# Performance work log

Hardware: AMD Instinct MI355X
Metric: run time of the kernel (lower is better)

## Reference

```python
import jax, jax.numpy as jnp
import numpy as np
from jax import lax

B, T, D, L = 64, 512, 1024, 32


def setup_inputs() -> dict:
    key = jax.random.key(0)
    ks = jax.random.split(key, 6)
    embeddings = jax.random.normal(ks[0], (B, T, D), dtype=jnp.float32)
    W = jax.random.normal(ks[1], (L, D), dtype=jnp.float32) * (1.0 / np.sqrt(D))
    b = jnp.zeros((L,), dtype=jnp.float32)
    start_trans = jax.random.normal(ks[2], (L,), dtype=jnp.float32) * 0.1
    end_trans = jax.random.normal(ks[3], (L,), dtype=jnp.float32) * 0.1
    trans = jax.random.normal(ks[4], (L, L), dtype=jnp.float32) * 0.1
    labels = jax.random.randint(ks[5], (B, T), 0, L, dtype=jnp.int32)
    mask = jnp.ones((B, T), dtype=bool)  # torchcrf requires mask[:, 0] == True
    return {"embeddings": embeddings, "W": W, "b": b,
            "start_trans": start_trans, "end_trans": end_trans,
            "trans": trans, "labels": labels, "mask": mask}


def _crf_nll(emissions, labels, mask, start_trans, end_trans, trans):
    # emissions: [B, T, L]; torchcrf works time-first internally.
    em = jnp.transpose(emissions, (1, 0, 2))          # [T, B, L]
    tg = labels.T                                      # [T, B]
    mk_b = mask.T                                      # [T, B] bool
    mk_f = mk_b.astype(emissions.dtype)
    bidx = jnp.arange(em.shape[1])

    # ---- numerator: score of the gold tag path ----
    score0 = start_trans[tg[0]] + em[0, bidx, tg[0]]   # [B]

    def num_step(carry, inp):
        prev_tag, score = carry
        e_t, tag_t, m_b, m_f = inp
        step = trans[prev_tag, tag_t] + e_t[bidx, tag_t]
        score = score + step * m_f
        prev_tag = jnp.where(m_b, tag_t, prev_tag)
        return (prev_tag, score), None

    (last_tag, num), _ = lax.scan(num_step, (tg[0], score0),
                                  (em[1:], tg[1:], mk_b[1:], mk_f[1:]))
    num = num + end_trans[last_tag]

    # ---- denominator: forward algorithm (log partition) ----
    alpha0 = start_trans[None, :] + em[0]              # [B, L]

    def den_step(alpha, inp):
        e_t, m_b = inp
        # alpha[b, i] + trans[i, j] + e_t[b, j] -> logsumexp over i
        nxt = jax.nn.logsumexp(alpha[:, :, None] + trans[None, :, :]
                               + e_t[:, None, :], axis=1)
        alpha = jnp.where(m_b[:, None], nxt, alpha)
        return alpha, None

    alpha, _ = lax.scan(den_step, alpha0, (em[1:], mk_b[1:]))
    den = jax.nn.logsumexp(alpha + end_trans[None, :], axis=1)  # [B]

    llh = num - den                                    # log-likelihood per seq
    return -jnp.mean(llh)                              # reduction='mean', negated


def reference(embeddings, W, b, start_trans, end_trans, trans, labels, mask):
    # dropout is identity at eval time
    emissions = jnp.einsum('btd,ld->btl', embeddings, W) + b  # [B, T, L]
    return _crf_nll(emissions, labels, mask, start_trans, end_trans, trans)
```

## Files before the change

### kernel.cpp

```cpp
#include <hip/hip_runtime.h>
#include <hip/hip_bf16.h>

#define NB 64
#define NT 512
#define ND 1024
#define NL 32
#define SEG 16
#define NSEG 32

typedef __attribute__((ext_vector_type(8)))  short bf16x8;
typedef __attribute__((ext_vector_type(4)))  float f32x4;
typedef __attribute__((ext_vector_type(16))) float f32x16;

__device__ __forceinline__ unsigned short bfh(float x) {
    __hip_bfloat16 h = __float2bfloat16(x);
    return *(unsigned short*)&h;
}
__device__ __forceinline__ float frombf(unsigned short u) {
    return __uint_as_float(((unsigned)u) << 16);
}

__global__ __launch_bounds__(256) void wb_kernel(
    const float* __restrict__ W, unsigned short* __restrict__ Wb)
{
    int i = blockIdx.x * 256 + threadIdx.x;
    float4 v = ((const float4*)W)[i];
    ushort4 o;
    o.x = bfh(v.x); o.y = bfh(v.y); o.z = bfh(v.z); o.w = bfh(v.w);
    ((ushort4*)Wb)[i] = o;
}

__global__ __launch_bounds__(256) void emis_kernel(
    const float* __restrict__ emb,
    const unsigned short* __restrict__ Wb,
    const float* __restrict__ bias,
    float* __restrict__ eme)
{
    __shared__ unsigned short As[64][80];
    const int tid  = threadIdx.x;
    const int wv   = tid >> 6;
    const int lane = tid & 63;
    const int m    = lane & 15;
    const int quad = lane >> 4;
    const int row0 = blockIdx.x * 64;

    const int srow = tid >> 4;
    const int sk4  = tid & 15;
    const float* gp = emb + (size_t)(row0 + srow) * ND + sk4 * 4;

    float4 rA[4];
#pragma unroll
    for (int q = 0; q < 4; q++) rA[q] = *(const float4*)(gp + (size_t)q * 16 * ND);

    f32x4 acc0 = {0.f, 0.f, 0.f, 0.f};
    f32x4 acc1 = {0.f, 0.f, 0.f, 0.f};

    for (int c = 0; c < 16; c++) {
        if (c) __syncthreads();
#pragma unroll
        for (int q = 0; q < 4; q++) {
            ushort4 pk;
            pk.x = bfh(rA[q].x); pk.y = bfh(rA[q].y);
            pk.z = bfh(rA[q].z); pk.w = bfh(rA[q].w);
            *(ushort4*)&As[srow + 16 * q][sk4 * 4] = pk;
        }
        __syncthreads();

        if (c < 15) {
            const float* np = gp + (c + 1) * 64;
#pragma unroll
            for (int q = 0; q < 4; q++) rA[q] = *(const float4*)(np + (size_t)q * 16 * ND);
        }

#pragma unroll
        for (int ks = 0; ks < 2; ks++) {
            int kb = c * 64 + ks * 32 + quad * 8;
            bf16x8 bf0 = *(const bf16x8*)&Wb[(size_t)m * ND + kb];
            bf16x8 bf1 = *(const bf16x8*)&Wb[(size_t)(16 + m) * ND + kb];
            bf16x8 af  = *(const bf16x8*)&As[16 * wv + m][ks * 32 + quad * 8];
            acc0 = __builtin_amdgcn_mfma_f32_16x16x32_bf16(af, bf0, acc0, 0, 0, 0);
            acc1 = __builtin_amdgcn_mfma_f32_16x16x32_bf16(af, bf1, acc1, 0, 0, 0);
        }
    }

    const int n = m;
    const float bl0 = bias[n];
    const float bl1 = bias[16 + n];
#pragma unroll
    for (int r = 0; r < 4; r++) {
        int R = row0 + 16 * wv + quad * 4 + r;
        float* op = eme + (size_t)R * NL;
        op[n]      = __expf(acc0[r] + bl0);
        op[16 + n] = __expf(acc1[r] + bl1);
    }
}

__global__ __launch_bounds__(64) void seg_kernel(
    const float* __restrict__ eme,
    const float* __restrict__ trans,
    const int*   __restrict__ labels,
    unsigned short* __restrict__ Pm,
    int*   __restrict__ exps,
    float* __restrict__ numpart)
{
    const int blk  = blockIdx.x;
    const int b    = blk >> 5;
    const int s    = blk & 31;
    const int lane = threadIdx.x;
    const int col  = lane & 31;
    const int h    = lane >> 5;
    const int t0   = s * SEG;
    const int tstart = (s == 0) ? 1 : t0;

    __shared__ __align__(16) float em_lds[SEG][NL];
    __shared__ __align__(16) unsigned short T2[2][32][40];

    {
        const float* src = eme + ((size_t)b * NT + t0) * NL;
        *(float4*)&((float*)em_lds)[lane * 8]     = *(const float4*)&src[lane * 8];
        *(float4*)&((float*)em_lds)[lane * 8 + 4] = *(const float4*)&src[lane * 8 + 4];
    }
    __syncthreads();

    {
        float npart = 0.f;
        if (lane < SEG) {
            int t = t0 + lane;
            if (t >= 1) {
                int pt = labels[b * NT + t - 1], ct = labels[b * NT + t];
                npart = trans[pt * NL + ct] + __logf(em_lds[lane][ct]);
            }
        }
#pragma unroll
        for (int mk = 32; mk >= 1; mk >>= 1) npart += __shfl_xor(npart, mk, 64);
        if (lane == 0) numpart[b * NSEG + s] = npart;
    }

    float Ecol[16];
#pragma unroll
    for (int j = 0; j < 8; j++) Ecol[j]     = __expf(trans[(8 * h + j) * NL + col]);
#pragma unroll
    for (int j = 0; j < 8; j++) Ecol[8 + j] = __expf(trans[(16 + 8 * h + j) * NL + col]);

    bf16x8 A1, A2;
    {
        const float* emt = em_lds[tstart - t0];
#pragma unroll
        for (int j = 0; j < 8; j++) {
            int k1 = 8 * h + j, k2 = 16 + 8 * h + j;
            ((unsigned short*)&A1)[j] = bfh(__expf(trans[col * NL + k1]) * emt[k1]);
            ((unsigned short*)&A2)[j] = bfh(__expf(trans[col * NL + k2]) * emt[k2]);
        }
    }

    int eseg = 0, par = 0, lastp = 0;
    for (int t = tstart + 1; t <= t0 + SEG - 1; t++) {
        float emn = em_lds[t - t0][col];
        bf16x8 B1, B2;
#pragma unroll
        for (int j = 0; j < 8; j++) {
            ((unsigned short*)&B1)[j] = bfh(Ecol[j] * emn);
            ((unsigned short*)&B2)[j] = bfh(Ecol[8 + j] * emn);
        }

        f32x16 acc;
#pragma unroll
        for (int i = 0; i < 16; i++) acc[i] = 0.f;
        acc = __builtin_amdgcn_mfma_f32_32x32x16_bf16(A1, B1, acc, 0, 0, 0);
        acc = __builtin_amdgcn_mfma_f32_32x32x16_bf16(A2, B2, acc, 0, 0, 0);

        int bits = __builtin_amdgcn_readlane(__float_as_int(acc[0]), 0);
        int e = (bits >> 23) & 255;
        eseg += e - 127;
        float scale = __uint_as_float((unsigned)(254 - e) << 23);

#pragma unroll
        for (int r = 0; r < 16; r++) {
            int row = (r & 3) + 8 * (r >> 2) + 4 * h;
            T2[par][row][col] = bfh(acc[r] * scale);
        }
        __syncthreads();
        A1 = *(const bf16x8*)&T2[par][col][8 * h];
        A2 = *(const bf16x8*)&T2[par][col][16 + 8 * h];
        lastp = par;
        par ^= 1;
    }

    if (h == 0) {
        unsigned short* dst = Pm + ((size_t)(b * NSEG + s) << 10) + col * 32;
        const uint4* srcrow = (const uint4*)&T2[lastp][col][0];
        ((uint4*)dst)[0] = srcrow[0];
        ((uint4*)dst)[1] = srcrow[1];
    }
    if (lane == 0) exps[b * NSEG + s] = eseg;
}

__global__ __launch_bounds__(64) void comb_kernel(
    const float* __restrict__ eme,
    const float* __restrict__ start_trans,
    const float* __restrict__ end_trans,
    const unsigned short* __restrict__ Pm,
    const int*   __restrict__ exps,
    const float* __restrict__ numpart,
    const int*   __restrict__ labels,
    float* __restrict__ den_out,
    float* __restrict__ num_out)
{
    const int b    = blockIdx.x;
    const int lane = threadIdx.x;
    const int col  = lane & 31;

    float a = __expf(start_trans[col]) * eme[(size_t)b * NT * NL + col];
    int sexp = 0;
    float sv[32];
#pragma unroll
    for (int i = 0; i < 32; i++)
        sv[i] = __int_as_float(__builtin_amdgcn_readlane(__float_as_int(a), i));

    const unsigned short* Pb = Pm + ((size_t)b * NSEG << 10);
    float Pc[32];
#pragma unroll
    for (int i = 0; i < 32; i++) Pc[i] = frombf(Pb[i * 32 + col]);

    for (int s = 0; s < NSEG; s++) {
        unsigned short nb[32];
        if (s + 1 < NSEG) {
            const unsigned short* q = Pb + ((s + 1) << 10);
#pragma unroll
            for (int i = 0; i < 32; i++) nb[i] = q[i * 32 + col];
        } else {
#pragma unroll
            for (int i = 0; i < 32; i++) nb[i] = 0;
        }

        float p0 = sv[0] * Pc[0], p1 = sv[1] * Pc[1];
        float p2 = sv[2] * Pc[2], p3 = sv[3] * Pc[3];
        float p4 = sv[4] * Pc[4], p5 = sv[5] * Pc[5];
        float p6 = sv[6] * Pc[6], p7 = sv[7] * Pc[7];
#pragma unroll
        for (int i = 8; i < 32; i += 8) {
            p0 = fmaf(sv[i + 0], Pc[i + 0], p0);
            p1 = fmaf(sv[i + 1], Pc[i + 1], p1);
            p2 = fmaf(sv[i + 2], Pc[i + 2], p2);
            p3 = fmaf(sv[i + 3], Pc[i + 3], p3);
            p4 = fmaf(sv[i + 4], Pc[i + 4], p4);
            p5 = fmaf(sv[i + 5], Pc[i + 5], p5);
            p6 = fmaf(sv[i + 6], Pc[i + 6], p6);
            p7 = fmaf(sv[i + 7], Pc[i + 7], p7);
        }
        a = (((p0 + p1) + (p2 + p3)) + ((p4 + p5) + (p6 + p7)));

        int bits = __builtin_amdgcn_readlane(__float_as_int(a), 0);
        int e = (bits >> 23) & 255;
        sexp += e - 127;
        a *= __uint_as_float((unsigned)(254 - e) << 23);

#pragma unroll
        for (int i = 0; i < 32; i++)
            sv[i] = __int_as_float(__builtin_amdgcn_readlane(__float_as_int(a), i));
#pragma unroll
        for (int i = 0; i < 32; i++) Pc[i] = frombf(nb[i]);
    }

    float sege = (lane < NSEG) ? (float)exps[b * NSEG + lane] : 0.f;
#pragma unroll
    for (int mk = 32; mk >= 1; mk >>= 1) sege += __shfl_xor(sege, mk, 64);

    float x = a * __expf(end_trans[col]);
#pragma unroll
    for (int mk = 16; mk >= 1; mk >>= 1) x += __shfl_xor(x, mk, 32);

    float nsum = (lane < NSEG) ? numpart[b * NSEG + lane] : 0.f;
#pragma unroll
    for (int mk = 32; mk >= 1; mk >>= 1) nsum += __shfl_xor(nsum, mk, 64);

    if (lane == 0) {
        int l0 = labels[b * NT], lT = labels[b * NT + NT - 1];
        num_out[b] = nsum + start_trans[l0]
                   + __logf(eme[(size_t)b * NT * NL + l0]) + end_trans[lT];
        den_out[b] = __logf(x)
                   + 0.69314718055994531f * ((float)sexp + sege);
    }
}

__global__ __launch_bounds__(64) void fin_kernel(
    const float* __restrict__ den, const float* __restrict__ num,
    float* __restrict__ out)
{
    int lane = threadIdx.x;
    float v = den[lane] - num[lane];
#pragma unroll
    for (int mk = 32; mk >= 1; mk >>= 1) v += __shfl_xor(v, mk, 64);
    if (lane == 0) out[0] = v * (1.0f / 64.0f);
}

extern "C" void kernel_launch(void* const* d_in, const int* in_sizes, int n_in,
                              void* d_out, int out_size, void* d_ws, size_t ws_size,
                              hipStream_t stream)
{
    const float* emb    = (const float*)d_in[0];
    const float* W      = (const float*)d_in[1];
    const float* bias   = (const float*)d_in[2];
    const float* st     = (const float*)d_in[3];
    const float* en     = (const float*)d_in[4];
    const float* tr     = (const float*)d_in[5];
    const int*   labels = (const int*)d_in[6];

    char* p = (char*)d_ws;
    float* eme = (float*)p;                 p += (size_t)NB * NT * NL * 4;
    unsigned short* Pm = (unsigned short*)p; p += (size_t)NB * NSEG * 1024 * 2;
    int*   exps = (int*)p;                  p += NB * NSEG * 4;
    float* nump = (float*)p;                p += NB * NSEG * 4;
    float* den  = (float*)p;                p += NB * 4;
    float* num  = (float*)p;                p += NB * 4;
    unsigned short* Wb = (unsigned short*)p;
    float* out = (float*)d_out;

    wb_kernel  <<<(NL * ND) / 1024, 256, 0, stream>>>(W, Wb);
    emis_kernel<<<(NB * NT) / 64, 256, 0, stream>>>(emb, Wb, bias, eme);
    seg_kernel <<<NB * NSEG, 64, 0, stream>>>(eme, tr, labels, Pm, exps, nump);
    comb_kernel<<<NB, 64, 0, stream>>>(eme, st, en, Pm, exps, nump, labels, den, num);
    fin_kernel <<<1, 64, 0, stream>>>(den, num, out);
}
```

Baseline: 246.8 us.

## Split-K emission GEMM with double-buffered LDS; bf16x3 segment products

The emission GEMM now uses 32-row blocks with a 2-way split over K across waves, double-buffered LDS staging and an LDS reduction. This doubles the grid size and cuts one barrier per iteration. Separately, the segment transfer-matrix products now use a hi/lo bf16 split (three MFMA pairs per step), and the segment matrices are stored as fp32 instead of bf16. The precision change triples the MFMA work in the sequential segment chain and doubles Pm traffic in exchange for accuracy.

```diff
diff --git a/kernel.cpp b/kernel.cpp
--- a/kernel.cpp
+++ b/kernel.cpp
@@ -36,62 +36,80 @@
     const float* __restrict__ bias,
     float* __restrict__ eme)
 {
-    __shared__ unsigned short As[64][80];
+    __shared__ unsigned short As[2][32][72];
+    __shared__ float red[2][2][64][8];
+
     const int tid  = threadIdx.x;
     const int wv   = tid >> 6;
     const int lane = tid & 63;
     const int m    = lane & 15;
     const int quad = lane >> 4;
-    const int row0 = blockIdx.x * 64;
-
-    const int srow = tid >> 4;
-    const int sk4  = tid & 15;
-    const float* gp = emb + (size_t)(row0 + srow) * ND + sk4 * 4;
-
-    float4 rA[4];
-#pragma unroll
-    for (int q = 0; q < 4; q++) rA[q] = *(const float4*)(gp + (size_t)q * 16 * ND);
+    const int rp   = wv & 1;
+    const int kh   = wv >> 1;
+    const int row0 = blockIdx.x * 32;
+
+    const int sr = tid >> 4;
+    const int c4 = tid & 15;
+    const float* gp0 = emb + (size_t)(row0 + sr) * ND + c4 * 4;
+    const float* gp1 = emb + (size_t)(row0 + 16 + sr) * ND + c4 * 4;
+
+    {
+        float4 r0 = *(const float4*)gp0;
+        float4 r1 = *(const float4*)gp1;
+        ushort4 p0, p1;
+        p0.x = bfh(r0.x); p0.y = bfh(r0.y); p0.z = bfh(r0.z); p0.w = bfh(r0.w);
+        p1.x = bfh(r1.x); p1.y = bfh(r1.y); p1.z = bfh(r1.z); p1.w = bfh(r1.w);
+        *(ushort4*)&As[0][sr][c4 * 4]      = p0;
+        *(ushort4*)&As[0][16 + sr][c4 * 4] = p1;
+    }
+    __syncthreads();
 
     f32x4 acc0 = {0.f, 0.f, 0.f, 0.f};
     f32x4 acc1 = {0.f, 0.f, 0.f, 0.f};
 
     for (int c = 0; c < 16; c++) {
-        if (c) __syncthreads();
-#pragma unroll
-        for (int q = 0; q < 4; q++) {
-            ushort4 pk;
-            pk.x = bfh(rA[q].x); pk.y = bfh(rA[q].y);
-            pk.z = bfh(rA[q].z); pk.w = bfh(rA[q].w);
-            *(ushort4*)&As[srow + 16 * q][sk4 * 4] = pk;
-        }
-        __syncthreads();
-
+        const int cur = c & 1;
+        float4 n0, n1;
         if (c < 15) {
-            const float* np = gp + (c + 1) * 64;
-#pragma unroll
-            for (int q = 0; q < 4; q++) rA[q] = *(const float4*)(np + (size_t)q * 16 * ND);
-        }
-
-#pragma unroll
-        for (int ks = 0; ks < 2; ks++) {
-            int kb = c * 64 + ks * 32 + quad * 8;
-            bf16x8 bf0 = *(const bf16x8*)&Wb[(size_t)m * ND + kb];
-            bf16x8 bf1 = *(const bf16x8*)&Wb[(size_t)(16 + m) * ND + kb];
-            bf16x8 af  = *(const bf16x8*)&As[16 * wv + m][ks * 32 + quad * 8];
-            acc0 = __builtin_amdgcn_mfma_f32_16x16x32_bf16(af, bf0, acc0, 0, 0, 0);
-            acc1 = __builtin_amdgcn_mfma_f32_16x16x32_bf16(af, bf1, acc1, 0, 0, 0);
-        }
-    }
-
-    const int n = m;
-    const float bl0 = bias[n];
-    const float bl1 = bias[16 + n];
-#pragma unroll
-    for (int r = 0; r < 4; r++) {
-        int R = row0 + 16 * wv + quad * 4 + r;
-        float* op = eme + (size_t)R * NL;
-        op[n]      = __expf(acc0[r] + bl0);
-        op[16 + n] = __expf(acc1[r] + bl1);
+            n0 = *(const float4*)(gp0 + (c + 1) * 64);
+            n1 = *(const float4*)(gp1 + (c + 1) * 64);
+        }
+
+        int kb = c * 64 + kh * 32 + quad * 8;
+        bf16x8 af  = *(const bf16x8*)&As[cur][rp * 16 + m][kh * 32 + quad * 8];
+        bf16x8 bf0 = *(const bf16x8*)&Wb[(size_t)m * ND + kb];
+        bf16x8 bf1 = *(const bf16x8*)&Wb[(size_t)(16 + m) * ND + kb];
+        acc0 = __builtin_amdgcn_mfma_f32_16x16x32_bf16(af, bf0, acc0, 0, 0, 0);
+        acc1 = __builtin_amdgcn_mfma_f32_16x16x32_bf16(af, bf1, acc1, 0, 0, 0);
+
+        if (c < 15) {
+            ushort4 q0, q1;
+            q0.x = bfh(n0.x); q0.y = bfh(n0.y); q0.z = bfh(n0.z); q0.w = bfh(n0.w);
+            q1.x = bfh(n1.x); q1.y = bfh(n1.y); q1.z = bfh(n1.z); q1.w = bfh(n1.w);
+            *(ushort4*)&As[cur ^ 1][sr][c4 * 4]      = q0;
+            *(ushort4*)&As[cur ^ 1][16 + sr][c4 * 4] = q1;
+            __syncthreads();
+        }
+    }
+
+#pragma unroll
+    for (int i = 0; i < 4; i++) red[kh][rp][lane][i]     = acc0[i];
+#pragma unroll
+    for (int i = 0; i < 4; i++) red[kh][rp][lane][4 + i] = acc1[i];
+    __syncthreads();
+
+    if (kh == 0) {
+        const float bl0 = bias[m];
+        const float bl1 = bias[16 + m];
+#pragma unroll
+        for (int r = 0; r < 4; r++) {
+            int R = row0 + rp * 16 + quad * 4 + r;
+            float* op = eme + (size_t)R * NL;
+            float v0 = red[0][rp][lane][r]     + red[1][rp][lane][r]     + bl0;
+            float v1 = red[0][rp][lane][4 + r] + red[1][rp][lane][4 + r] + bl1;
+            op[m]      = __expf(v0);
+            op[16 + m] = __expf(v1);
+        }
     }
 }
 
@@ -99,7 +117,7 @@
     const float* __restrict__ eme,
     const float* __restrict__ trans,
     const int*   __restrict__ labels,
-    unsigned short* __restrict__ Pm,
+    float* __restrict__ Pm,
     int*   __restrict__ exps,
     float* __restrict__ numpart)
 {
@@ -113,7 +131,8 @@
     const int tstart = (s == 0) ? 1 : t0;
 
     __shared__ __align__(16) float em_lds[SEG][NL];
-    __shared__ __align__(16) unsigned short T2[2][32][40];
+    __shared__ __align__(16) unsigned short Thi[2][32][40];
+    __shared__ __align__(16) unsigned short Tlo[2][32][40];
 
     {
         const float* src = eme + ((size_t)b * NT + t0) * NL;
@@ -142,55 +161,76 @@
 #pragma unroll
     for (int j = 0; j < 8; j++) Ecol[8 + j] = __expf(trans[(16 + 8 * h + j) * NL + col]);
 
-    bf16x8 A1, A2;
+    bf16x8 Ah1, Ah2, Al1, Al2;
     {
         const float* emt = em_lds[tstart - t0];
 #pragma unroll
         for (int j = 0; j < 8; j++) {
             int k1 = 8 * h + j, k2 = 16 + 8 * h + j;
-            ((unsigned short*)&A1)[j] = bfh(__expf(trans[col * NL + k1]) * emt[k1]);
-            ((unsigned short*)&A2)[j] = bfh(__expf(trans[col * NL + k2]) * emt[k2]);
-        }
-    }
-
-    int eseg = 0, par = 0, lastp = 0;
-    for (int t = tstart + 1; t <= t0 + SEG - 1; t++) {
+            float v1 = __expf(trans[col * NL + k1]) * emt[k1];
+            float v2 = __expf(trans[col * NL + k2]) * emt[k2];
+            unsigned short h1 = bfh(v1), h2 = bfh(v2);
+            ((unsigned short*)&Ah1)[j] = h1;
+            ((unsigned short*)&Ah2)[j] = h2;
+            ((unsigned short*)&Al1)[j] = bfh(v1 - frombf(h1));
+            ((unsigned short*)&Al2)[j] = bfh(v2 - frombf(h2));
+        }
+    }
+
+    int eseg = 0, par = 0;
+    const int tlast = t0 + SEG - 1;
+    for (int t = tstart + 1; t <= tlast; t++) {
         float emn = em_lds[t - t0][col];
-        bf16x8 B1, B2;
+        bf16x8 Bh1, Bh2, Bl1, Bl2;
 #pragma unroll
         for (int j = 0; j < 8; j++) {
-            ((unsigned short*)&B1)[j] = bfh(Ecol[j] * emn);
-            ((unsigned short*)&B2)[j] = bfh(Ecol[8 + j] * emn);
+            float v1 = Ecol[j] * emn;
+            float v2 = Ecol[8 + j] * emn;
+            unsigned short h1 = bfh(v1), h2 = bfh(v2);
+            ((unsigned short*)&Bh1)[j] = h1;
+            ((unsigned short*)&Bh2)[j] = h2;
+            ((unsigned short*)&Bl1)[j] = bfh(v1 - frombf(h1));
+            ((unsigned short*)&Bl2)[j] = bfh(v2 - frombf(h2));
         }
 
         f32x16 acc;
 #pragma unroll
         for (int i = 0; i < 16; i++) acc[i] = 0.f;
-        acc = __builtin_amdgcn_mfma_f32_32x32x16_bf16(A1, B1, acc, 0, 0, 0);
-        acc = __builtin_amdgcn_mfma_f32_32x32x16_bf16(A2, B2, acc, 0, 0, 0);
+        acc = __builtin_amdgcn_mfma_f32_32x32x16_bf16(Ah1, Bh1, acc, 0, 0, 0);
+        acc = __builtin_amdgcn_mfma_f32_32x32x16_bf16(Ah2, Bh2, acc, 0, 0, 0);
+        acc = __builtin_amdgcn_mfma_f32_32x32x16_bf16(Ah1, Bl1, acc, 0, 0, 0);
+        acc = __builtin_amdgcn_mfma_f32_32x32x16_bf16(Ah2, Bl2, acc, 0, 0, 0);
+        acc = __builtin_amdgcn_mfma_f32_32x32x16_bf16(Al1, Bh1, acc, 0, 0, 0);
+        acc = __builtin_amdgcn_mfma_f32_32x32x16_bf16(Al2, Bh2, acc, 0, 0, 0);
 
         int bits = __builtin_amdgcn_readlane(__float_as_int(acc[0]), 0);
         int e = (bits >> 23) & 255;
         eseg += e - 127;
         float scale = __uint_as_float((unsigned)(254 - e) << 23);
 
-#pragma unroll
-        for (int r = 0; r < 16; r++) {
-            int row = (r & 3) + 8 * (r >> 2) + 4 * h;
-            T2[par][row][col] = bfh(acc[r] * scale);
-        }
-        __syncthreads();
-        A1 = *(const bf16x8*)&T2[par][col][8 * h];
-        A2 = *(const bf16x8*)&T2[par][col][16 + 8 * h];
-        lastp = par;
-        par ^= 1;
-    }
-
-    if (h == 0) {
-        unsigned short* dst = Pm + ((size_t)(b * NSEG + s) << 10) + col * 32;
-        const uint4* srcrow = (const uint4*)&T2[lastp][col][0];
-        ((uint4*)dst)[0] = srcrow[0];
-        ((uint4*)dst)[1] = srcrow[1];
+        if (t < tlast) {
+#pragma unroll
+            for (int r = 0; r < 16; r++) {
+                int row = (r & 3) + 8 * (r >> 2) + 4 * h;
+                float v = acc[r] * scale;
+                unsigned short hi = bfh(v);
+                Thi[par][row][col] = hi;
+                Tlo[par][row][col] = bfh(v - frombf(hi));
+            }
+            __syncthreads();
+            Ah1 = *(const bf16x8*)&Thi[par][col][8 * h];
+            Ah2 = *(const bf16x8*)&Thi[par][col][16 + 8 * h];
+            Al1 = *(const bf16x8*)&Tlo[par][col][8 * h];
+            Al2 = *(const bf16x8*)&Tlo[par][col][16 + 8 * h];
+            par ^= 1;
+        } else {
+            float* dst = Pm + ((size_t)(b * NSEG + s) << 10);
+#pragma unroll
+            for (int r = 0; r < 16; r++) {
+                int row = (r & 3) + 8 * (r >> 2) + 4 * h;
+                dst[row * 32 + col] = acc[r] * scale;
+            }
+        }
     }
     if (lane == 0) exps[b * NSEG + s] = eseg;
 }
@@ -199,7 +239,7 @@
     const float* __restrict__ eme,
     const float* __restrict__ start_trans,
     const float* __restrict__ end_trans,
-    const unsigned short* __restrict__ Pm,
+    const float* __restrict__ Pm,
     const int*   __restrict__ exps,
     const float* __restrict__ numpart,
     const int*   __restrict__ labels,
@@ -217,20 +257,20 @@
     for (int i = 0; i < 32; i++)
         sv[i] = __int_as_float(__builtin_amdgcn_readlane(__float_as_int(a), i));
 
-    const unsigned short* Pb = Pm + ((size_t)b * NSEG << 10);
+    const float* Pb = Pm + ((size_t)b * NSEG << 10);
     float Pc[32];
 #pragma unroll
-    for (int i = 0; i < 32; i++) Pc[i] = frombf(Pb[i * 32 + col]);
+    for (int i = 0; i < 32; i++) Pc[i] = Pb[i * 32 + col];
 
     for (int s = 0; s < NSEG; s++) {
-        unsigned short nb[32];
+        float nb[32];
         if (s + 1 < NSEG) {
-            const unsigned short* q = Pb + ((s + 1) << 10);
+            const float* q = Pb + ((s + 1) << 10);
 #pragma unroll
             for (int i = 0; i < 32; i++) nb[i] = q[i * 32 + col];
         } else {
 #pragma unroll
-            for (int i = 0; i < 32; i++) nb[i] = 0;
+            for (int i = 0; i < 32; i++) nb[i] = 0.f;
         }
 
         float p0 = sv[0] * Pc[0], p1 = sv[1] * Pc[1];
@@ -259,7 +299,7 @@
         for (int i = 0; i < 32; i++)
             sv[i] = __int_as_float(__builtin_amdgcn_readlane(__float_as_int(a), i));
 #pragma unroll
-        for (int i = 0; i < 32; i++) Pc[i] = frombf(nb[i]);
+        for (int i = 0; i < 32; i++) Pc[i] = nb[i];
     }
 
     float sege = (lane < NSEG) ? (float)exps[b * NSEG + lane] : 0.f;
@@ -307,17 +347,17 @@
     const int*   labels = (const int*)d_in[6];
 
     char* p = (char*)d_ws;
-    float* eme = (float*)p;                 p += (size_t)NB * NT * NL * 4;
-    unsigned short* Pm = (unsigned short*)p; p += (size_t)NB * NSEG * 1024 * 2;
-    int*   exps = (int*)p;                  p += NB * NSEG * 4;
-    float* nump = (float*)p;                p += NB * NSEG * 4;
-    float* den  = (float*)p;                p += NB * 4;
-    float* num  = (float*)p;                p += NB * 4;
+    float* eme = (float*)p;                  p += (size_t)NB * NT * NL * 4;
+    float* Pm  = (float*)p;                  p += (size_t)NB * NSEG * 1024 * 4;
+    int*   exps = (int*)p;                   p += NB * NSEG * 4;
+    float* nump = (float*)p;                 p += NB * NSEG * 4;
+    float* den  = (float*)p;                 p += NB * 4;
+    float* num  = (float*)p;                 p += NB * 4;
     unsigned short* Wb = (unsigned short*)p;
     float* out = (float*)d_out;
 
     wb_kernel  <<<(NL * ND) / 1024, 256, 0, stream>>>(W, Wb);
-    emis_kernel<<<(NB * NT) / 64, 256, 0, stream>>>(emb, Wb, bias, eme);
+    emis_kernel<<<(NB * NT) / 32, 256, 0, stream>>>(emb, Wb, bias, eme);
     seg_kernel <<<NB * NSEG, 64, 0, stream>>>(eme, tr, labels, Pm, exps, nump);
     comb_kernel<<<NB, 64, 0, stream>>>(eme, st, en, Pm, exps, nump, labels, den, num);
     fin_kernel <<<1, 64, 0, stream>>>(den, num, out);
```

Measured after the change: 251.1 us. No clear change (+1.7%).
